# Kernel tuning notes

Hardware: AMD Instinct MI355X
Metric: run time of the kernel (lower is better)

## Reference

```python
import jax, jax.numpy as jnp
import numpy as np

P = 2; NH = 16; HS = 1024; NL = 12; NC = 1000
B, D, H, W = 32, 64, 32, 32
LFEAT = P * P * D  # 256 per-patch feature dim


def _sincos_1d(dim, pos):
    omega = np.arange(dim // 2, dtype=np.float64) / (dim / 2.0)
    omega = 1.0 / 10000 ** omega
    out = np.einsum('m,d->md', pos.reshape(-1), omega)
    return np.concatenate([np.sin(out), np.cos(out)], axis=1)


def _pos_embed(dim, grid_size):
    g = np.arange(grid_size, dtype=np.float32)
    grid = np.stack(np.meshgrid(g, g), axis=0).reshape(2, 1, grid_size, grid_size)
    emb = np.concatenate([_sincos_1d(dim // 2, grid[0]), _sincos_1d(dim // 2, grid[1])], axis=1)
    return jnp.asarray(emb, dtype=jnp.float32)


def setup_inputs() -> dict:
    key = jax.random.key(0)
    ks = iter(jax.random.split(key, 40))
    def w(shape, s=0.02):
        return jax.random.normal(next(ks), shape, jnp.float32) * s
    return {
        'x': jax.random.normal(next(ks), (B, D, H, W), jnp.float32),
        'y': jax.random.randint(next(ks), (B,), 0, NC),
        't': jax.random.randint(next(ks), (B,), 0, 1000),
        'proj_w': w((LFEAT, HS)), 'proj_b': jnp.zeros((HS,), jnp.float32),
        'pos_embed': _pos_embed(HS, H // P),
        'emb_table': w((NC + 1, HS)),
        'blk_mod_w': w((NL, HS, 6 * HS)), 'blk_mod_b': jnp.zeros((NL, 6 * HS), jnp.float32),
        'blk_wq': w((NL, HS, HS)), 'blk_bq': jnp.zeros((NL, HS), jnp.float32),
        'blk_wk': w((NL, HS, HS)), 'blk_bk': jnp.zeros((NL, HS), jnp.float32),
        'blk_wv': w((NL, HS, HS)), 'blk_bv': jnp.zeros((NL, HS), jnp.float32),
        'blk_wo': w((NL, HS, HS)), 'blk_bo': jnp.zeros((NL, HS), jnp.float32),
        'blk_fc1_w': w((NL, HS, 4 * HS)), 'blk_fc1_b': jnp.zeros((NL, 4 * HS), jnp.float32),
        'blk_fc2_w': w((NL, 4 * HS, HS)), 'blk_fc2_b': jnp.zeros((NL, HS), jnp.float32),
        'fin_mod_w': w((HS, 2 * HS)), 'fin_mod_b': jnp.zeros((2 * HS,), jnp.float32),
        'fin_out_w': w((HS, LFEAT)), 'fin_out_b': jnp.zeros((LFEAT,), jnp.float32),
    }


def _ln(z):
    mu = jnp.mean(z, -1, keepdims=True)
    var = jnp.mean((z - mu) ** 2, -1, keepdims=True)
    return (z - mu) * jax.lax.rsqrt(var + 1e-5)


def _forward(x, y, t, proj_w, proj_b, pos_embed, emb_table,
             blk_mod_w, blk_mod_b, blk_wq, blk_bq, blk_wk, blk_bk, blk_wv, blk_bv,
             blk_wo, blk_bo, blk_fc1_w, blk_fc1_b, blk_fc2_w, blk_fc2_b,
             fin_mod_w, fin_mod_b, fin_out_w, fin_out_b):
    Bc, Dc, Hc, Wc = x.shape
    Hp, Wp = Hc // P, Wc // P
    dh = HS // NH
    # patchify_flatten: (B, L, P*P*D)
    tok = x.reshape(Bc, Dc, Hp, P, Wp, P).transpose(0, 2, 4, 3, 5, 1).reshape(Bc, Hp * Wp, P * P * Dc)
    tok = tok @ proj_w + proj_b + pos_embed[None]
    # timestep_embedding: [cos, sin] order per source
    half = HS // 2
    freqs = jnp.exp(-jnp.log(jnp.float32(10000.0)) * jnp.arange(half, dtype=jnp.float32) / half)
    ang = t.astype(jnp.float32)[:, None] * freqs[None]
    c = jnp.concatenate([jnp.cos(ang), jnp.sin(ang)], axis=-1) + emb_table[y]
    c_act = jax.nn.silu(c)  # each block applies silu to c (c is not mutated across blocks)

    def block(xc, p):
        mw, mb, wq, bq, wk, bk, wv, bv, wo, bo, f1w, f1b, f2w, f2b = p
        mod = c_act @ mw + mb
        sh_a, sc_a, g_a, sh_m, sc_m, g_m = jnp.split(mod, 6, axis=1)
        hx = _ln(xc) * (1 + sc_a[:, None]) + sh_a[:, None]
        def heads(z, wz, bz):
            return (z @ wz + bz).reshape(Bc, -1, NH, dh).transpose(0, 2, 1, 3)
        q, k, v = heads(hx, wq, bq), heads(hx, wk, bk), heads(hx, wv, bv)
        logits = jnp.einsum('bhqd,bhkd->bhqk', q, k) / jnp.sqrt(jnp.float32(dh))
        # non-AR mask buffer is all zeros -> no-op
        attn = jax.nn.softmax(logits, axis=-1)
        o = jnp.einsum('bhqk,bhkd->bhqd', attn, v).transpose(0, 2, 1, 3).reshape(Bc, -1, HS)
        xc = xc + g_a[:, None] * (o @ wo + bo)
        hx = _ln(xc) * (1 + sc_m[:, None]) + sh_m[:, None]
        mlp = jax.nn.gelu(hx @ f1w + f1b, approximate=False) @ f2w + f2b
        return xc + g_m[:, None] * mlp, None

    tok, _ = jax.lax.scan(block, tok, (blk_mod_w, blk_mod_b, blk_wq, blk_bq, blk_wk, blk_bk,
                                       blk_wv, blk_bv, blk_wo, blk_bo,
                                       blk_fc1_w, blk_fc1_b, blk_fc2_w, blk_fc2_b))
    fmod = c_act @ fin_mod_w + fin_mod_b
    sh, sc = jnp.split(fmod, 2, axis=1)
    out = (_ln(tok) * (1 + sc[:, None]) + sh[:, None]) @ fin_out_w + fin_out_b
    # unpatchify -> (B, D, H, W)
    return out.reshape(Bc, Hp, Wp, P, P, Dc).transpose(0, 5, 1, 3, 2, 4).reshape(Bc, Dc, Hc, Wc)


def reference(x, y, t, proj_w, proj_b, pos_embed, emb_table,
              blk_mod_w, blk_mod_b, blk_wq, blk_bq, blk_wk, blk_bk, blk_wv, blk_bv,
              blk_wo, blk_bo, blk_fc1_w, blk_fc1_b, blk_fc2_w, blk_fc2_b,
              fin_mod_w, fin_mod_b, fin_out_w, fin_out_b):
    return _forward(x, y, t, proj_w, proj_b, pos_embed, emb_table,
                    blk_mod_w, blk_mod_b, blk_wq, blk_bq, blk_wk, blk_bk, blk_wv, blk_bv,
                    blk_wo, blk_bo, blk_fc1_w, blk_fc1_b, blk_fc2_w, blk_fc2_b,
                    fin_mod_w, fin_mod_b, fin_out_w, fin_out_b)
```

## Files before the change

kernel.cpp:

```cpp
#include <hip/hip_runtime.h>
#include <hip/hip_bf16.h>
#include <math.h>

typedef short s16x8 __attribute__((ext_vector_type(8)));
typedef float f32x4 __attribute__((ext_vector_type(4)));
typedef unsigned short u16;

#define BAR() __builtin_amdgcn_s_barrier()
#define PRIO1() __builtin_amdgcn_s_setprio(1)
#define PRIO0() __builtin_amdgcn_s_setprio(0)
#define VMCNT0() asm volatile("s_waitcnt vmcnt(0)" ::: "memory")

__device__ __forceinline__ u16 f2b(float f) {
    unsigned u = __builtin_bit_cast(unsigned, f);
    u += 0x7fffu + ((u >> 16) & 1u);
    return (u16)(u >> 16);
}
__device__ __forceinline__ f32x4 mfma16(s16x8 a, s16x8 b, f32x4 c) {
    return __builtin_amdgcn_mfma_f32_16x16x32_bf16(a, b, c, 0, 0, 0);
}
__device__ __forceinline__ void gload16(const void* g, void* l) {
    __builtin_amdgcn_global_load_lds((const __attribute__((address_space(1))) unsigned*)g,
                                     (__attribute__((address_space(3))) unsigned*)l, 16, 0, 0);
}

__global__ __launch_bounds__(256) void patchify_kernel(const float* __restrict__ x, u16* __restrict__ out) {
    int idx = blockIdx.x * 256 + threadIdx.x;
    int row = idx >> 8, col = idx & 255;
    int b = row >> 8, ll = row & 255, hp = ll >> 4, wp = ll & 15;
    int pp = col >> 6, d = col & 63;
    out[idx] = f2b(x[(size_t)((b * 64 + d) * 32 + hp * 2 + (pp >> 1)) * 32 + wp * 2 + (pp & 1)]);
}

__global__ __launch_bounds__(256) void cact_kernel(const int* __restrict__ t, const int* __restrict__ y,
                                                   const float* __restrict__ emb, float* __restrict__ cactF) {
    int b = blockIdx.x, tid = threadIdx.x;
    float tv = (float)t[b];
    int yb = y[b];
#pragma unroll
    for (int j = 0; j < 4; ++j) {
        int c = tid * 4 + j;
        int f = (c < 512) ? c : c - 512;
        float freq = __expf(-9.210340371976184f * (float)f * (1.f / 512.f));
        float ang = tv * freq;
        float v = (c < 512) ? cosf(ang) : sinf(ang);
        v += emb[(size_t)yb * 1024 + c];
        v = v / (1.f + __expf(-v));
        cactF[b * 1024 + c] = v;
    }
}

__global__ __launch_bounds__(256) void bcat_kernel(const float* __restrict__ bq, const float* __restrict__ bk,
                                                   const float* __restrict__ bv, float* __restrict__ out) {
    int lyr = blockIdx.x, j = blockIdx.y, tid = threadIdx.x;
    const float* src = (j == 0) ? bq : ((j == 1) ? bk : bv);
    float4 v = ((const float4*)(src + (size_t)lyr * 1024))[tid];
    ((float4*)(out + (size_t)lyr * 3072 + j * 1024))[tid] = v;
}

__global__ __launch_bounds__(256) void mod32_kernel(const float* __restrict__ cactF, const float* __restrict__ W,
                                                    const float* __restrict__ bias, float* __restrict__ out, int N) {
    __shared__ float cs[32 * 256];
    __shared__ float red[4 * 32 * 64];
    int tid = threadIdx.x, lane = tid & 63, kg = tid >> 6;
    int n = blockIdx.x * 64 + lane;
    float acc[32];
#pragma unroll
    for (int r = 0; r < 32; ++r) acc[r] = 0.f;
    for (int ch = 0; ch < 4; ++ch) {
        __syncthreads();
#pragma unroll
        for (int j = 0; j < 8; ++j) {
            int idx = tid * 4 + j * 1024;
            float4 v = *(const float4*)&cactF[(size_t)(idx >> 8) * 1024 + ch * 256 + (idx & 255)];
            *(float4*)&cs[idx] = v;
        }
        __syncthreads();
        const float* Wp = W + (size_t)(ch * 256 + kg * 64) * N + n;
        for (int kk = 0; kk < 64; kk += 4) {
            float w0 = Wp[(size_t)(kk + 0) * N];
            float w1 = Wp[(size_t)(kk + 1) * N];
            float w2 = Wp[(size_t)(kk + 2) * N];
            float w3 = Wp[(size_t)(kk + 3) * N];
            int kb = kg * 64 + kk;
#pragma unroll
            for (int r = 0; r < 32; ++r) {
                float4 cv = *(const float4*)&cs[r * 256 + kb];
                acc[r] += cv.x * w0 + cv.y * w1 + cv.z * w2 + cv.w * w3;
            }
        }
    }
#pragma unroll
    for (int r = 0; r < 32; ++r) red[(kg * 32 + r) * 64 + lane] = acc[r];
    __syncthreads();
    int r = tid >> 3, j0 = (tid & 7) * 8;
#pragma unroll
    for (int jj = 0; jj < 8; ++jj) {
        int nn = j0 + jj;
        float s = red[(0 * 32 + r) * 64 + nn] + red[(1 * 32 + r) * 64 + nn] +
                  red[(2 * 32 + r) * 64 + nn] + red[(3 * 32 + r) * 64 + nn];
        out[(size_t)r * N + blockIdx.x * 64 + nn] = s + bias[blockIdx.x * 64 + nn];
    }
}

__device__ __forceinline__ void tpose_body(float (*tile)[65], const float* __restrict__ in,
                                           u16* __restrict__ out, int R, int C, int r0, int c0, int tid) {
    int rr = tid >> 4, cc = (tid & 15) * 4;
#pragma unroll
    for (int j = 0; j < 4; ++j) {
        float4 v = *(const float4*)&in[(size_t)(r0 + j * 16 + rr) * C + c0 + cc];
        tile[j * 16 + rr][cc]     = v.x;
        tile[j * 16 + rr][cc + 1] = v.y;
        tile[j * 16 + rr][cc + 2] = v.z;
        tile[j * 16 + rr][cc + 3] = v.w;
    }
    __syncthreads();
    int oc = tid >> 3, r8 = (tid & 7) * 8;
#pragma unroll
    for (int j = 0; j < 2; ++j) {
        int ocl = j * 32 + oc;
        s16x8 vv;
#pragma unroll
        for (int e = 0; e < 8; ++e) vv[e] = (short)f2b(tile[r8 + e][ocl]);
        *(s16x8*)&out[(size_t)(c0 + ocl) * R + r0 + r8] = vv;
    }
}

__global__ __launch_bounds__(256) void transpose_cvt64k(const float* __restrict__ in, u16* __restrict__ out,
                                                        int R, int C) {
    __shared__ float tile[64][65];
    tpose_body(tile, in, out, R, C, blockIdx.y * 64, blockIdx.x * 64, threadIdx.x);
}

__global__ __launch_bounds__(256) void transpose_layer(
    const float* __restrict__ wq, const float* __restrict__ wk,
    const float* __restrict__ wv, const float* __restrict__ wo, const float* __restrict__ f1,
    const float* __restrict__ f2,
    u16* __restrict__ qkvT, u16* __restrict__ woT, u16* __restrict__ f1T, u16* __restrict__ f2T) {
    __shared__ float tile[64][65];
    int bid = blockIdx.x, tid = threadIdx.x;
    const float* src; u16* dst; int R, C, tloc;
    if (bid < 256)       { src = wq; dst = qkvT;               R = 1024; C = 1024; tloc = bid; }
    else if (bid < 512)  { src = wk; dst = qkvT + 1024 * 1024; R = 1024; C = 1024; tloc = bid - 256; }
    else if (bid < 768)  { src = wv; dst = qkvT + 2048 * 1024; R = 1024; C = 1024; tloc = bid - 512; }
    else if (bid < 1024) { src = wo; dst = woT;                R = 1024; C = 1024; tloc = bid - 768; }
    else if (bid < 2048) { src = f1; dst = f1T;                R = 1024; C = 4096; tloc = bid - 1024; }
    else                 { src = f2; dst = f2T;                R = 4096; C = 1024; tloc = bid - 2048; }
    int tx = C >> 6;
    int ty = tloc / tx, txi = tloc - ty * tx;
    tpose_body(tile, src, dst, R, C, ty * 64, txi * 64, tid);
}

__global__ __launch_bounds__(256) void ln_mod_kernel(const float* __restrict__ x, const float* __restrict__ modv,
                                                     int mod_ld, int sh_off, int sc_off, u16* __restrict__ out) {
    int row = blockIdx.x, tid = threadIdx.x, b = row >> 8;
    float4 xv = ((const float4*)(x + (size_t)row * 1024))[tid];
    float s = xv.x + xv.y + xv.z + xv.w;
    float s2 = xv.x * xv.x + xv.y * xv.y + xv.z * xv.z + xv.w * xv.w;
#pragma unroll
    for (int d = 1; d < 64; d <<= 1) { s += __shfl_xor(s, d); s2 += __shfl_xor(s2, d); }
    __shared__ float red[8];
    int w = tid >> 6;
    if ((tid & 63) == 0) { red[w] = s; red[4 + w] = s2; }
    __syncthreads();
    s = red[0] + red[1] + red[2] + red[3];
    s2 = red[4] + red[5] + red[6] + red[7];
    float mu = s * (1.f / 1024.f);
    float rs = rsqrtf(s2 * (1.f / 1024.f) - mu * mu + 1e-5f);
    const float* shp = modv + (size_t)b * mod_ld + sh_off;
    const float* scp = modv + (size_t)b * mod_ld + sc_off;
    float4 sh4 = ((const float4*)shp)[tid];
    float4 sc4 = ((const float4*)scp)[tid];
    u16 o0 = f2b((xv.x - mu) * rs * (1.f + sc4.x) + sh4.x);
    u16 o1 = f2b((xv.y - mu) * rs * (1.f + sc4.y) + sh4.y);
    u16 o2 = f2b((xv.z - mu) * rs * (1.f + sc4.z) + sh4.z);
    u16 o3 = f2b((xv.w - mu) * rs * (1.f + sc4.w) + sh4.w);
    unsigned long long pk = (unsigned long long)o0 | ((unsigned long long)o1 << 16) |
                            ((unsigned long long)o2 << 32) | ((unsigned long long)o3 << 48);
    *(unsigned long long*)&out[(size_t)row * 1024 + tid * 4] = pk;
}

template <int EPI>
__global__ __launch_bounds__(512, 1) void gemm8(
    const u16* __restrict__ A, int lda, const u16* __restrict__ Bt, int ldb,
    int M, int N, int K, const float* __restrict__ bias,
    float* __restrict__ outF, u16* __restrict__ outB, int ldc,
    const float* __restrict__ aux1, const float* __restrict__ aux2, int gateOff) {
    __shared__ u16 As[3][256 * 64];
    __shared__ u16 Bs[3][128 * 64];

    const int tid = threadIdx.x, w = tid >> 6, l = tid & 63;
    const int wm = w >> 1, wn = w & 1;

    const int nbn = N >> 7;
    const int orig = blockIdx.x;
    const int cpx = gridDim.x >> 3;
    const int wg = (orig & 7) * cpx + (orig >> 3);
    const int bm = wg / nbn, bn = wg - bm * nbn;
    const int row0 = bm << 8, col0 = bn << 7;

    const int NT = K >> 6;

    const int srow = tid >> 3, sslot = tid & 7;
    const int ksl = sslot ^ (srow & 7);
    const u16* gA = A + (size_t)(row0 + srow) * lda + ksl * 8;
    const u16* gB = Bt + (size_t)(col0 + srow) * ldb + ksl * 8;
    const int lOff = srow * 64 + sslot * 8;

    const int fr = l & 15, fg = l >> 4;
    const int arow = wm * 64 + fr;
    const int brow = wn * 64 + fr;

    f32x4 acc[4][4];
#pragma unroll
    for (int m = 0; m < 4; ++m)
#pragma unroll
        for (int n = 0; n < 4; ++n) acc[m][n] = (f32x4){0.f, 0.f, 0.f, 0.f};

    {
        u16* a0 = &As[0][lOff];
        u16* b0 = &Bs[0][lOff];
#pragma unroll
        for (int a = 0; a < 4; ++a) gload16(gA + (size_t)a * 64 * lda, a0 + a * 4096);
#pragma unroll
        for (int b = 0; b < 2; ++b) gload16(gB + (size_t)b * 64 * ldb, b0 + b * 4096);
        if (NT > 1) {
            u16* a1 = &As[1][lOff];
#pragma unroll
            for (int a = 0; a < 3; ++a) gload16(gA + (size_t)a * 64 * lda + 64, a1 + a * 4096);
        }
    }
    if (NT > 1) { asm volatile("s_waitcnt vmcnt(3)" ::: "memory"); }
    else        { VMCNT0(); }
    BAR();
    __builtin_amdgcn_sched_barrier(0);

    int q = 0;
    for (int t = 0; t < NT; ++t) {
        const u16* ca = As[q];
        const u16* cb = Bs[q];
        const int q1 = (q == 2) ? 0 : q + 1;
        const int q2 = (q1 == 2) ? 0 : q1 + 1;

        s16x8 af[4][2], bf[4][2];
#pragma unroll
        for (int m = 0; m < 4; ++m) {
            int r = arow + m * 16;
            af[m][0] = *(const s16x8*)(ca + r * 64 + ((fg     ^ (r & 7)) * 8));
            af[m][1] = *(const s16x8*)(ca + r * 64 + (((4 + fg) ^ (r & 7)) * 8));
        }
#pragma unroll
        for (int n = 0; n < 2; ++n) {
            int r = brow + n * 16;
            bf[n][0] = *(const s16x8*)(cb + r * 64 + ((fg     ^ (r & 7)) * 8));
            bf[n][1] = *(const s16x8*)(cb + r * 64 + (((4 + fg) ^ (r & 7)) * 8));
        }
        if (t + 1 < NT) {
            gload16(gA + (size_t)(3 * 64) * lda + (size_t)(t + 1) * 64, &As[q1][lOff] + 3 * 4096);
            gload16(gB + (size_t)(t + 1) * 64, &Bs[q1][lOff]);
            gload16(gB + (size_t)(1 * 64) * ldb + (size_t)(t + 1) * 64, &Bs[q1][lOff] + 4096);
        }
        BAR(); PRIO1();
#pragma unroll
        for (int m = 0; m < 4; ++m)
#pragma unroll
            for (int n = 0; n < 2; ++n) {
                acc[m][n] = mfma16(af[m][0], bf[n][0], acc[m][n]);
                acc[m][n] = mfma16(af[m][1], bf[n][1], acc[m][n]);
            }
        PRIO0(); BAR();
#pragma unroll
        for (int n = 0; n < 2; ++n) {
            int r = brow + (n + 2) * 16;
            bf[n + 2][0] = *(const s16x8*)(cb + r * 64 + ((fg     ^ (r & 7)) * 8));
            bf[n + 2][1] = *(const s16x8*)(cb + r * 64 + (((4 + fg) ^ (r & 7)) * 8));
        }
        if (t + 2 < NT) {
#pragma unroll
            for (int a = 0; a < 3; ++a)
                gload16(gA + (size_t)a * 64 * lda + (size_t)(t + 2) * 64, &As[q2][lOff] + a * 4096);
        }
        BAR(); PRIO1();
#pragma unroll
        for (int m = 0; m < 4; ++m)
#pragma unroll
            for (int n = 2; n < 4; ++n) {
                acc[m][n] = mfma16(af[m][0], bf[n][0], acc[m][n]);
                acc[m][n] = mfma16(af[m][1], bf[n][1], acc[m][n]);
            }
        PRIO0();
        if (t < NT - 2)       { asm volatile("s_waitcnt vmcnt(3)" ::: "memory"); }
        else if (t == NT - 2) { VMCNT0(); }
        if (t < NT - 1) {
            BAR();
            __builtin_amdgcn_sched_barrier(0);
        }
        q = q1;
    }

    const int erow = row0 + wm * 64 + fg * 4;
    const int ecol = col0 + wn * 64 + fr;
#pragma unroll
    for (int m = 0; m < 4; ++m) {
#pragma unroll
        for (int n = 0; n < 4; ++n) {
#pragma unroll
            for (int r = 0; r < 4; ++r) {
                int row = erow + m * 16 + r;
                int col = ecol + n * 16;
                float v = acc[m][n][r];
                if constexpr (EPI == 1) {
                    outB[(size_t)row * ldc + col] = f2b(v + bias[col]);
                } else if constexpr (EPI == 2) {
                    outF[(size_t)row * ldc + col] = v + bias[col] + aux1[(size_t)(row & 255) * 1024 + col];
                } else if constexpr (EPI == 3) {
                    outF[(size_t)row * ldc + col] =
                        aux1[(size_t)row * ldc + col] +
                        aux2[(size_t)(row >> 8) * 6144 + gateOff + col] * (v + bias[col]);
                } else {
                    float xg = v + bias[col];
                    outB[(size_t)row * ldc + col] = f2b(0.5f * xg * (1.f + erff(xg * 0.70710678118654752f)));
                }
            }
        }
    }
}

__global__ __launch_bounds__(256, 2) void gemm_fin(
    const u16* __restrict__ A, int lda, const u16* __restrict__ Bt, int ldb,
    int M, int N, int K, const float* __restrict__ bias, float* outF) {
    __shared__ u16 Asl[128 * 32];
    __shared__ u16 Bsl[128 * 32];
    const int tid = threadIdx.x, w = tid >> 6, l = tid & 63;
    const int row0 = blockIdx.y * 128, col0 = blockIdx.x * 128;
    const int wm = w >> 1, wn = w & 1;

    f32x4 acc[4][4];
#pragma unroll
    for (int m = 0; m < 4; ++m)
#pragma unroll
        for (int n = 0; n < 4; ++n) acc[m][n] = (f32x4){0.f, 0.f, 0.f, 0.f};

    const int rA0 = w * 16 + (l >> 2), rA1 = rA0 + 64;
    const int kc = (l & 3) * 8;
    const u16* a0 = A + (size_t)(row0 + rA0) * lda + kc;
    const u16* a1 = A + (size_t)(row0 + rA1) * lda + kc;
    const u16* b0 = Bt + (size_t)(col0 + rA0) * ldb + kc;
    const u16* b1 = Bt + (size_t)(col0 + rA1) * ldb + kc;
    u16* la0 = &Asl[rA0 * 32 + kc];
    u16* la1 = &Asl[rA1 * 32 + kc];
    u16* lb0 = &Bsl[rA0 * 32 + kc];
    u16* lb1 = &Bsl[rA1 * 32 + kc];

    for (int k0 = 0; k0 < K; k0 += 32) {
        __syncthreads();
        gload16(a0 + k0, la0);
        gload16(a1 + k0, la1);
        gload16(b0 + k0, lb0);
        gload16(b1 + k0, lb1);
        __syncthreads();
        s16x8 af[4], bfr[4];
#pragma unroll
        for (int m = 0; m < 4; ++m)
            af[m] = *(const s16x8*)&Asl[(wm * 64 + m * 16 + (l & 15)) * 32 + (l >> 4) * 8];
#pragma unroll
        for (int n = 0; n < 4; ++n)
            bfr[n] = *(const s16x8*)&Bsl[(wn * 64 + n * 16 + (l & 15)) * 32 + (l >> 4) * 8];
#pragma unroll
        for (int m = 0; m < 4; ++m)
#pragma unroll
            for (int n = 0; n < 4; ++n) acc[m][n] = mfma16(af[m], bfr[n], acc[m][n]);
    }

#pragma unroll
    for (int m = 0; m < 4; ++m) {
#pragma unroll
        for (int n = 0; n < 4; ++n) {
#pragma unroll
            for (int r = 0; r < 4; ++r) {
                int row = row0 + wm * 64 + m * 16 + (l >> 4) * 4 + r;
                int col = col0 + wn * 64 + n * 16 + (l & 15);
                float xg = acc[m][n][r] + bias[col];
                int bb = row >> 8, ll = row & 255, hp = ll >> 4, wp = ll & 15;
                int pp = col >> 6, d = col & 63;
                outF[(size_t)((bb * 64 + d) * 32 + hp * 2 + (pp >> 1)) * 32 + wp * 2 + (pp & 1)] = xg;
            }
        }
    }
}

__global__ __launch_bounds__(256, 2) void attn_kernel(const u16* __restrict__ qkv, u16* __restrict__ obuf) {
    __shared__ u16 Qs[64 * 64];
    __shared__ u16 Ks[256 * 64];
    __shared__ u16 VTs[64 * 256];
    int qt = blockIdx.x, h = blockIdx.y, b = blockIdx.z;
    int tid = threadIdx.x, w = tid >> 6, l = tid & 63;
    size_t base = (size_t)b * 256 * 3072;

    {
        int r = tid >> 2;
#pragma unroll
        for (int j = 0; j < 2; ++j) {
            int sg = (tid & 3) + j * 4;
            *(s16x8*)&Qs[r * 64 + sg * 8] =
                *(const s16x8*)&qkv[base + (size_t)(qt * 64 + r) * 3072 + h * 64 + sg * 8];
        }
    }
#pragma unroll
    for (int j = 0; j < 8; ++j) {
        int i = tid + j * 256;
        int r = i >> 3, sg = i & 7;
        *(s16x8*)&Ks[r * 64 + sg * 8] =
            *(const s16x8*)&qkv[base + (size_t)r * 3072 + 1024 + h * 64 + sg * 8];
    }
#pragma unroll
    for (int j = 0; j < 8; ++j) {
        int i = tid + j * 256;
        int r = i >> 3, sg = i & 7;
        s16x8 v = *(const s16x8*)&qkv[base + (size_t)r * 3072 + 2048 + h * 64 + sg * 8];
#pragma unroll
        for (int e = 0; e < 8; ++e) VTs[(sg * 8 + e) * 256 + r] = ((const u16*)&v)[e];
    }
    __syncthreads();

    s16x8 aq0 = *(const s16x8*)&Qs[(w * 16 + (l & 15)) * 64 + (l >> 4) * 8];
    s16x8 aq1 = *(const s16x8*)&Qs[(w * 16 + (l & 15)) * 64 + 32 + (l >> 4) * 8];
    f32x4 sf[16];
#pragma unroll
    for (int cf = 0; cf < 16; ++cf) {
        f32x4 a = (f32x4){0.f, 0.f, 0.f, 0.f};
        s16x8 bk0 = *(const s16x8*)&Ks[(cf * 16 + (l & 15)) * 64 + (l >> 4) * 8];
        s16x8 bk1 = *(const s16x8*)&Ks[(cf * 16 + (l & 15)) * 64 + 32 + (l >> 4) * 8];
        a = mfma16(aq0, bk0, a);
        a = mfma16(aq1, bk1, a);
        sf[cf] = a * 0.125f;
    }
    __syncthreads();

#pragma unroll
    for (int r = 0; r < 4; ++r) {
        float m = -1e30f;
#pragma unroll
        for (int cf = 0; cf < 16; ++cf) m = fmaxf(m, sf[cf][r]);
#pragma unroll
        for (int d = 1; d < 16; d <<= 1) m = fmaxf(m, __shfl_xor(m, d));
        float sm = 0.f;
#pragma unroll
        for (int cf = 0; cf < 16; ++cf) { float e = __expf(sf[cf][r] - m); sf[cf][r] = e; sm += e; }
#pragma unroll
        for (int d = 1; d < 16; d <<= 1) sm += __shfl_xor(sm, d);
        float inv = 1.f / sm;
        int rl = w * 16 + (l >> 4) * 4 + r;
#pragma unroll
        for (int cf = 0; cf < 16; ++cf) Ks[rl * 256 + cf * 16 + (l & 15)] = f2b(sf[cf][r] * inv);
    }
    __syncthreads();

    f32x4 oacc[4];
#pragma unroll
    for (int cf = 0; cf < 4; ++cf) oacc[cf] = (f32x4){0.f, 0.f, 0.f, 0.f};
#pragma unroll
    for (int ks = 0; ks < 8; ++ks) {
        s16x8 ap = *(const s16x8*)&Ks[(w * 16 + (l & 15)) * 256 + ks * 32 + (l >> 4) * 8];
#pragma unroll
        for (int cf = 0; cf < 4; ++cf) {
            s16x8 bv = *(const s16x8*)&VTs[(cf * 16 + (l & 15)) * 256 + ks * 32 + (l >> 4) * 8];
            oacc[cf] = mfma16(ap, bv, oacc[cf]);
        }
    }
    size_t orow0 = (size_t)(b * 256 + qt * 64 + w * 16);
#pragma unroll
    for (int cf = 0; cf < 4; ++cf)
#pragma unroll
        for (int r = 0; r < 4; ++r) {
            int rr = (l >> 4) * 4 + r;
            obuf[(orow0 + rr) * 1024 + h * 64 + cf * 16 + (l & 15)] = f2b(oacc[cf][r]);
        }
}

extern "C" void kernel_launch(void* const* d_in, const int* in_sizes, int n_in,
                              void* d_out, int out_size, void* d_ws, size_t ws_size,
                              hipStream_t stream) {
    (void)in_sizes; (void)n_in; (void)out_size; (void)ws_size;
    const float* x         = (const float*)d_in[0];
    const int*   y         = (const int*)d_in[1];
    const int*   t         = (const int*)d_in[2];
    const float* proj_w    = (const float*)d_in[3];
    const float* proj_b    = (const float*)d_in[4];
    const float* pos_embed = (const float*)d_in[5];
    const float* emb_table = (const float*)d_in[6];
    const float* blk_mod_w = (const float*)d_in[7];
    const float* blk_mod_b = (const float*)d_in[8];
    const float* blk_wq    = (const float*)d_in[9];
    const float* blk_bq    = (const float*)d_in[10];
    const float* blk_wk    = (const float*)d_in[11];
    const float* blk_bk    = (const float*)d_in[12];
    const float* blk_wv    = (const float*)d_in[13];
    const float* blk_bv    = (const float*)d_in[14];
    const float* blk_wo    = (const float*)d_in[15];
    const float* blk_bo    = (const float*)d_in[16];
    const float* blk_f1w   = (const float*)d_in[17];
    const float* blk_f1b   = (const float*)d_in[18];
    const float* blk_f2w   = (const float*)d_in[19];
    const float* blk_f2b   = (const float*)d_in[20];
    const float* fin_mod_w = (const float*)d_in[21];
    const float* fin_mod_b = (const float*)d_in[22];
    const float* fin_out_w = (const float*)d_in[23];
    const float* fin_out_b = (const float*)d_in[24];
    float* out = (float*)d_out;

    char* ws = (char*)d_ws;
    size_t off = 0;
    auto alloc = [&](size_t bytes) -> char* {
        char* p = ws + off;
        off += (bytes + 255) & ~(size_t)255;
        return p;
    };
    float* xc    = (float*)alloc(8192ull * 1024 * 4);
    u16*   hx    = (u16*)alloc(8192ull * 1024 * 2);
    u16*   qkvb  = (u16*)alloc(8192ull * 3072 * 2);
    u16*   obufp = (u16*)alloc(8192ull * 1024 * 2);
    u16*   h1    = (u16*)alloc(8192ull * 4096 * 2);
    u16*   patchA= (u16*)alloc(8192ull * 256 * 2);
    float* cactF = (float*)alloc(32ull * 1024 * 4);
    float* modb  = (float*)alloc(32ull * 6144 * 4);
    float* fmod  = (float*)alloc(32ull * 2048 * 4);
    float* bqkv  = (float*)alloc(12ull * 3072 * 4);
    u16*   projT = (u16*)alloc(1024ull * 256 * 2);
    u16*   foT   = (u16*)alloc(256ull * 1024 * 2);
    u16*   qkvT  = (u16*)alloc(3072ull * 1024 * 2);
    u16*   woT   = (u16*)alloc(1024ull * 1024 * 2);
    u16*   f1T   = (u16*)alloc(4096ull * 1024 * 2);
    u16*   f2T   = (u16*)alloc(1024ull * 4096 * 2);

    patchify_kernel<<<8192, 256, 0, stream>>>(x, patchA);
    cact_kernel<<<32, 256, 0, stream>>>(t, y, emb_table, cactF);
    bcat_kernel<<<dim3(12, 3), 256, 0, stream>>>(blk_bq, blk_bk, blk_bv, bqkv);
    transpose_cvt64k<<<dim3(16, 4), 256, 0, stream>>>(proj_w, projT, 256, 1024);
    transpose_cvt64k<<<dim3(4, 16), 256, 0, stream>>>(fin_out_w, foT, 1024, 256);
    mod32_kernel<<<32, 256, 0, stream>>>(cactF, fin_mod_w, fin_mod_b, fmod, 2048);

    gemm8<2><<<256, 512, 0, stream>>>(patchA, 256, projT, 256, 8192, 1024, 256,
                                      proj_b, xc, nullptr, 1024, pos_embed, nullptr, 0);

    for (int i = 0; i < 12; ++i) {
        transpose_layer<<<3072, 256, 0, stream>>>(
            blk_wq + (size_t)i * 1024 * 1024, blk_wk + (size_t)i * 1024 * 1024,
            blk_wv + (size_t)i * 1024 * 1024, blk_wo + (size_t)i * 1024 * 1024,
            blk_f1w + (size_t)i * 1024 * 4096, blk_f2w + (size_t)i * 4096 * 1024,
            qkvT, woT, f1T, f2T);

        mod32_kernel<<<96, 256, 0, stream>>>(cactF, blk_mod_w + (size_t)i * 1024 * 6144,
                                             blk_mod_b + (size_t)i * 6144, modb, 6144);
        ln_mod_kernel<<<8192, 256, 0, stream>>>(xc, modb, 6144, 0, 1024, hx);
        gemm8<1><<<768, 512, 0, stream>>>(hx, 1024, qkvT, 1024, 8192, 3072, 1024,
                                          bqkv + (size_t)i * 3072, nullptr, qkvb, 3072,
                                          nullptr, nullptr, 0);
        attn_kernel<<<dim3(4, 16, 32), 256, 0, stream>>>(qkvb, obufp);
        gemm8<3><<<256, 512, 0, stream>>>(obufp, 1024, woT, 1024, 8192, 1024, 1024,
                                          blk_bo + (size_t)i * 1024, xc, nullptr, 1024,
                                          xc, modb, 2048);
        ln_mod_kernel<<<8192, 256, 0, stream>>>(xc, modb, 6144, 3072, 4096, hx);
        gemm8<4><<<1024, 512, 0, stream>>>(hx, 1024, f1T, 1024, 8192, 4096, 1024,
                                           blk_f1b + (size_t)i * 4096, nullptr, h1, 4096,
                                           nullptr, nullptr, 0);
        gemm8<3><<<256, 512, 0, stream>>>(h1, 4096, f2T, 4096, 8192, 1024, 4096,
                                          blk_f2b + (size_t)i * 1024, xc, nullptr, 1024,
                                          xc, modb, 5120);
    }
    ln_mod_kernel<<<8192, 256, 0, stream>>>(xc, fmod, 2048, 0, 1024, hx);
    gemm_fin<<<dim3(2, 64), 256, 0, stream>>>(hx, 1024, foT, 1024, 8192, 256, 1024,
                                              fin_out_b, out);
}
```

Measured before the change: 5.576 ms.

## Replace 256x128 GEMM with 128x128 multi-occupancy kernel and batch weight transposes

The 512-thread 256x128x64 GEMM, with its priority-interleaved two-half schedule, is replaced by a 256-thread 128x128x32 kernel. It uses a triple-buffered global-to-LDS prefetch and launch bounds that allow 3 blocks per CU. The final-layer GEMM becomes an epilogue variant of the same kernel. All 12 layers' weight transposes now run in one upfront launch into per-layer buffers instead of one launch per layer, which removes serial per-layer transpose phases at the cost of more workspace. The smaller K-tile drops the LDS XOR swizzle, which risks bank conflicts and lower MFMA density per barrier.

```diff
diff --git a/kernel.cpp b/kernel.cpp
--- a/kernel.cpp
+++ b/kernel.cpp
@@ -7,8 +7,8 @@
 typedef unsigned short u16;
 
 #define BAR() __builtin_amdgcn_s_barrier()
-#define PRIO1() __builtin_amdgcn_s_setprio(1)
-#define PRIO0() __builtin_amdgcn_s_setprio(0)
+#define SCHEDB() __builtin_amdgcn_sched_barrier(0)
+#define VMCNT4() asm volatile("s_waitcnt vmcnt(4)" ::: "memory")
 #define VMCNT0() asm volatile("s_waitcnt vmcnt(0)" ::: "memory")
 
 __device__ __forceinline__ u16 f2b(float f) {
@@ -132,20 +132,24 @@
     tpose_body(tile, in, out, R, C, blockIdx.y * 64, blockIdx.x * 64, threadIdx.x);
 }
 
-__global__ __launch_bounds__(256) void transpose_layer(
+__global__ __launch_bounds__(256) void transpose_all(
     const float* __restrict__ wq, const float* __restrict__ wk,
-    const float* __restrict__ wv, const float* __restrict__ wo, const float* __restrict__ f1,
-    const float* __restrict__ f2,
+    const float* __restrict__ wv, const float* __restrict__ wo,
+    const float* __restrict__ f1, const float* __restrict__ f2,
     u16* __restrict__ qkvT, u16* __restrict__ woT, u16* __restrict__ f1T, u16* __restrict__ f2T) {
     __shared__ float tile[64][65];
-    int bid = blockIdx.x, tid = threadIdx.x;
+    int lyr = blockIdx.x / 3072;
+    int bid = blockIdx.x - lyr * 3072;
+    int tid = threadIdx.x;
+    const size_t sq = (size_t)lyr * 1024 * 1024;
+    const size_t sf = (size_t)lyr * 4096 * 1024;
     const float* src; u16* dst; int R, C, tloc;
-    if (bid < 256)       { src = wq; dst = qkvT;               R = 1024; C = 1024; tloc = bid; }
-    else if (bid < 512)  { src = wk; dst = qkvT + 1024 * 1024; R = 1024; C = 1024; tloc = bid - 256; }
-    else if (bid < 768)  { src = wv; dst = qkvT + 2048 * 1024; R = 1024; C = 1024; tloc = bid - 512; }
-    else if (bid < 1024) { src = wo; dst = woT;                R = 1024; C = 1024; tloc = bid - 768; }
-    else if (bid < 2048) { src = f1; dst = f1T;                R = 1024; C = 4096; tloc = bid - 1024; }
-    else                 { src = f2; dst = f2T;                R = 4096; C = 1024; tloc = bid - 2048; }
+    if (bid < 256)       { src = wq + sq; dst = qkvT + (size_t)lyr * 3072 * 1024;               R = 1024; C = 1024; tloc = bid; }
+    else if (bid < 512)  { src = wk + sq; dst = qkvT + (size_t)lyr * 3072 * 1024 + 1024 * 1024; R = 1024; C = 1024; tloc = bid - 256; }
+    else if (bid < 768)  { src = wv + sq; dst = qkvT + (size_t)lyr * 3072 * 1024 + 2048 * 1024; R = 1024; C = 1024; tloc = bid - 512; }
+    else if (bid < 1024) { src = wo + sq; dst = woT + sq;                                       R = 1024; C = 1024; tloc = bid - 768; }
+    else if (bid < 2048) { src = f1 + sf; dst = f1T + sf;                                       R = 1024; C = 4096; tloc = bid - 1024; }
+    else                 { src = f2 + sf; dst = f2T + sf;                                       R = 4096; C = 1024; tloc = bid - 2048; }
     int tx = C >> 6;
     int ty = tloc / tx, txi = tloc - ty * tx;
     tpose_body(tile, src, dst, R, C, ty * 64, txi * 64, tid);
@@ -181,35 +185,31 @@
 }
 
 template <int EPI>
-__global__ __launch_bounds__(512, 1) void gemm8(
+__global__ __launch_bounds__(256, 3) void gemm128p(
     const u16* __restrict__ A, int lda, const u16* __restrict__ Bt, int ldb,
     int M, int N, int K, const float* __restrict__ bias,
     float* __restrict__ outF, u16* __restrict__ outB, int ldc,
     const float* __restrict__ aux1, const float* __restrict__ aux2, int gateOff) {
-    __shared__ u16 As[3][256 * 64];
-    __shared__ u16 Bs[3][128 * 64];
+    __shared__ u16 As[3][128 * 32];
+    __shared__ u16 Bs[3][128 * 32];
 
     const int tid = threadIdx.x, w = tid >> 6, l = tid & 63;
     const int wm = w >> 1, wn = w & 1;
 
     const int nbn = N >> 7;
-    const int orig = blockIdx.x;
     const int cpx = gridDim.x >> 3;
-    const int wg = (orig & 7) * cpx + (orig >> 3);
+    const int wg = (blockIdx.x & 7) * cpx + (blockIdx.x >> 3);
     const int bm = wg / nbn, bn = wg - bm * nbn;
-    const int row0 = bm << 8, col0 = bn << 7;
-
-    const int NT = K >> 6;
-
-    const int srow = tid >> 3, sslot = tid & 7;
-    const int ksl = sslot ^ (srow & 7);
-    const u16* gA = A + (size_t)(row0 + srow) * lda + ksl * 8;
-    const u16* gB = Bt + (size_t)(col0 + srow) * ldb + ksl * 8;
-    const int lOff = srow * 64 + sslot * 8;
-
-    const int fr = l & 15, fg = l >> 4;
-    const int arow = wm * 64 + fr;
-    const int brow = wn * 64 + fr;
+    const int row0 = bm << 7, col0 = bn << 7;
+    const int NT = K >> 5;
+
+    const int rA0 = w * 16 + (l >> 2), rA1 = rA0 + 64;
+    const int kc = (l & 3) * 8;
+    const u16* a0 = A + (size_t)(row0 + rA0) * lda + kc;
+    const u16* a1 = A + (size_t)(row0 + rA1) * lda + kc;
+    const u16* b0 = Bt + (size_t)(col0 + rA0) * ldb + kc;
+    const u16* b1 = Bt + (size_t)(col0 + rA1) * ldb + kc;
+    const int lo0 = rA0 * 32 + kc, lo1 = rA1 * 32 + kc;
 
     f32x4 acc[4][4];
 #pragma unroll
@@ -217,97 +217,50 @@
 #pragma unroll
         for (int n = 0; n < 4; ++n) acc[m][n] = (f32x4){0.f, 0.f, 0.f, 0.f};
 
-    {
-        u16* a0 = &As[0][lOff];
-        u16* b0 = &Bs[0][lOff];
-#pragma unroll
-        for (int a = 0; a < 4; ++a) gload16(gA + (size_t)a * 64 * lda, a0 + a * 4096);
-#pragma unroll
-        for (int b = 0; b < 2; ++b) gload16(gB + (size_t)b * 64 * ldb, b0 + b * 4096);
-        if (NT > 1) {
-            u16* a1 = &As[1][lOff];
-#pragma unroll
-            for (int a = 0; a < 3; ++a) gload16(gA + (size_t)a * 64 * lda + 64, a1 + a * 4096);
-        }
-    }
-    if (NT > 1) { asm volatile("s_waitcnt vmcnt(3)" ::: "memory"); }
-    else        { VMCNT0(); }
-    BAR();
-    __builtin_amdgcn_sched_barrier(0);
+    gload16(a0, &As[0][lo0]); gload16(a1, &As[0][lo1]);
+    gload16(b0, &Bs[0][lo0]); gload16(b1, &Bs[0][lo1]);
+    if (NT > 1) {
+        gload16(a0 + 32, &As[1][lo0]); gload16(a1 + 32, &As[1][lo1]);
+        gload16(b0 + 32, &Bs[1][lo0]); gload16(b1 + 32, &Bs[1][lo1]);
+        VMCNT4();
+    } else {
+        VMCNT0();
+    }
+    BAR(); SCHEDB();
 
     int q = 0;
     for (int t = 0; t < NT; ++t) {
-        const u16* ca = As[q];
-        const u16* cb = Bs[q];
-        const int q1 = (q == 2) ? 0 : q + 1;
-        const int q2 = (q1 == 2) ? 0 : q1 + 1;
-
-        s16x8 af[4][2], bf[4][2];
-#pragma unroll
-        for (int m = 0; m < 4; ++m) {
-            int r = arow + m * 16;
-            af[m][0] = *(const s16x8*)(ca + r * 64 + ((fg     ^ (r & 7)) * 8));
-            af[m][1] = *(const s16x8*)(ca + r * 64 + (((4 + fg) ^ (r & 7)) * 8));
-        }
-#pragma unroll
-        for (int n = 0; n < 2; ++n) {
-            int r = brow + n * 16;
-            bf[n][0] = *(const s16x8*)(cb + r * 64 + ((fg     ^ (r & 7)) * 8));
-            bf[n][1] = *(const s16x8*)(cb + r * 64 + (((4 + fg) ^ (r & 7)) * 8));
-        }
-        if (t + 1 < NT) {
-            gload16(gA + (size_t)(3 * 64) * lda + (size_t)(t + 1) * 64, &As[q1][lOff] + 3 * 4096);
-            gload16(gB + (size_t)(t + 1) * 64, &Bs[q1][lOff]);
-            gload16(gB + (size_t)(1 * 64) * ldb + (size_t)(t + 1) * 64, &Bs[q1][lOff] + 4096);
-        }
-        BAR(); PRIO1();
+        int q2 = q + 2; if (q2 >= 3) q2 -= 3;
+        if (t + 2 < NT) {
+            int k2 = (t + 2) * 32;
+            gload16(a0 + k2, &As[q2][lo0]); gload16(a1 + k2, &As[q2][lo1]);
+            gload16(b0 + k2, &Bs[q2][lo0]); gload16(b1 + k2, &Bs[q2][lo1]);
+        }
+        s16x8 af[4], bfr[4];
 #pragma unroll
         for (int m = 0; m < 4; ++m)
-#pragma unroll
-            for (int n = 0; n < 2; ++n) {
-                acc[m][n] = mfma16(af[m][0], bf[n][0], acc[m][n]);
-                acc[m][n] = mfma16(af[m][1], bf[n][1], acc[m][n]);
-            }
-        PRIO0(); BAR();
-#pragma unroll
-        for (int n = 0; n < 2; ++n) {
-            int r = brow + (n + 2) * 16;
-            bf[n + 2][0] = *(const s16x8*)(cb + r * 64 + ((fg     ^ (r & 7)) * 8));
-            bf[n + 2][1] = *(const s16x8*)(cb + r * 64 + (((4 + fg) ^ (r & 7)) * 8));
-        }
-        if (t + 2 < NT) {
-#pragma unroll
-            for (int a = 0; a < 3; ++a)
-                gload16(gA + (size_t)a * 64 * lda + (size_t)(t + 2) * 64, &As[q2][lOff] + a * 4096);
-        }
-        BAR(); PRIO1();
+            af[m] = *(const s16x8*)&As[q][(wm * 64 + m * 16 + (l & 15)) * 32 + (l >> 4) * 8];
+#pragma unroll
+        for (int n = 0; n < 4; ++n)
+            bfr[n] = *(const s16x8*)&Bs[q][(wn * 64 + n * 16 + (l & 15)) * 32 + (l >> 4) * 8];
 #pragma unroll
         for (int m = 0; m < 4; ++m)
 #pragma unroll
-            for (int n = 2; n < 4; ++n) {
-                acc[m][n] = mfma16(af[m][0], bf[n][0], acc[m][n]);
-                acc[m][n] = mfma16(af[m][1], bf[n][1], acc[m][n]);
-            }
-        PRIO0();
-        if (t < NT - 2)       { asm volatile("s_waitcnt vmcnt(3)" ::: "memory"); }
-        else if (t == NT - 2) { VMCNT0(); }
-        if (t < NT - 1) {
-            BAR();
-            __builtin_amdgcn_sched_barrier(0);
-        }
-        q = q1;
-    }
-
-    const int erow = row0 + wm * 64 + fg * 4;
-    const int ecol = col0 + wn * 64 + fr;
+            for (int n = 0; n < 4; ++n) acc[m][n] = mfma16(af[m], bfr[n], acc[m][n]);
+        if (t + 2 < NT)      { VMCNT4(); }
+        else if (t + 1 < NT) { VMCNT0(); }
+        if (t + 1 < NT) { BAR(); SCHEDB(); }
+        q = q + 1; if (q >= 3) q -= 3;
+    }
+
 #pragma unroll
     for (int m = 0; m < 4; ++m) {
 #pragma unroll
         for (int n = 0; n < 4; ++n) {
 #pragma unroll
             for (int r = 0; r < 4; ++r) {
-                int row = erow + m * 16 + r;
-                int col = ecol + n * 16;
+                int row = row0 + wm * 64 + m * 16 + (l >> 4) * 4 + r;
+                int col = col0 + wn * 64 + n * 16 + (l & 15);
                 float v = acc[m][n][r];
                 if constexpr (EPI == 1) {
                     outB[(size_t)row * ldc + col] = f2b(v + bias[col]);
@@ -317,73 +270,15 @@
                     outF[(size_t)row * ldc + col] =
                         aux1[(size_t)row * ldc + col] +
                         aux2[(size_t)(row >> 8) * 6144 + gateOff + col] * (v + bias[col]);
+                } else if constexpr (EPI == 4) {
+                    float xg = v + bias[col];
+                    outB[(size_t)row * ldc + col] = f2b(0.5f * xg * (1.f + erff(xg * 0.70710678118654752f)));
                 } else {
                     float xg = v + bias[col];
-                    outB[(size_t)row * ldc + col] = f2b(0.5f * xg * (1.f + erff(xg * 0.70710678118654752f)));
+                    int bb = row >> 8, ll = row & 255, hp = ll >> 4, wp = ll & 15;
+                    int pp = col >> 6, d = col & 63;
+                    outF[(size_t)((bb * 64 + d) * 32 + hp * 2 + (pp >> 1)) * 32 + wp * 2 + (pp & 1)] = xg;
                 }
-            }
-        }
-    }
-}
-
-__global__ __launch_bounds__(256, 2) void gemm_fin(
-    const u16* __restrict__ A, int lda, const u16* __restrict__ Bt, int ldb,
-    int M, int N, int K, const float* __restrict__ bias, float* outF) {
-    __shared__ u16 Asl[128 * 32];
-    __shared__ u16 Bsl[128 * 32];
-    const int tid = threadIdx.x, w = tid >> 6, l = tid & 63;
-    const int row0 = blockIdx.y * 128, col0 = blockIdx.x * 128;
-    const int wm = w >> 1, wn = w & 1;
-
-    f32x4 acc[4][4];
-#pragma unroll
-    for (int m = 0; m < 4; ++m)
-#pragma unroll
-        for (int n = 0; n < 4; ++n) acc[m][n] = (f32x4){0.f, 0.f, 0.f, 0.f};
-
-    const int rA0 = w * 16 + (l >> 2), rA1 = rA0 + 64;
-    const int kc = (l & 3) * 8;
-    const u16* a0 = A + (size_t)(row0 + rA0) * lda + kc;
-    const u16* a1 = A + (size_t)(row0 + rA1) * lda + kc;
-    const u16* b0 = Bt + (size_t)(col0 + rA0) * ldb + kc;
-    const u16* b1 = Bt + (size_t)(col0 + rA1) * ldb + kc;
-    u16* la0 = &Asl[rA0 * 32 + kc];
-    u16* la1 = &Asl[rA1 * 32 + kc];
-    u16* lb0 = &Bsl[rA0 * 32 + kc];
-    u16* lb1 = &Bsl[rA1 * 32 + kc];
-
-    for (int k0 = 0; k0 < K; k0 += 32) {
-        __syncthreads();
-        gload16(a0 + k0, la0);
-        gload16(a1 + k0, la1);
-        gload16(b0 + k0, lb0);
-        gload16(b1 + k0, lb1);
-        __syncthreads();
-        s16x8 af[4], bfr[4];
-#pragma unroll
-        for (int m = 0; m < 4; ++m)
-            af[m] = *(const s16x8*)&Asl[(wm * 64 + m * 16 + (l & 15)) * 32 + (l >> 4) * 8];
-#pragma unroll
-        for (int n = 0; n < 4; ++n)
-            bfr[n] = *(const s16x8*)&Bsl[(wn * 64 + n * 16 + (l & 15)) * 32 + (l >> 4) * 8];
-#pragma unroll
-        for (int m = 0; m < 4; ++m)
-#pragma unroll
-            for (int n = 0; n < 4; ++n) acc[m][n] = mfma16(af[m], bfr[n], acc[m][n]);
-    }
-
-#pragma unroll
-    for (int m = 0; m < 4; ++m) {
-#pragma unroll
-        for (int n = 0; n < 4; ++n) {
-#pragma unroll
-            for (int r = 0; r < 4; ++r) {
-                int row = row0 + wm * 64 + m * 16 + (l >> 4) * 4 + r;
-                int col = col0 + wn * 64 + n * 16 + (l & 15);
-                float xg = acc[m][n][r] + bias[col];
-                int bb = row >> 8, ll = row & 255, hp = ll >> 4, wp = ll & 15;
-                int pp = col >> 6, d = col & 63;
-                outF[(size_t)((bb * 64 + d) * 32 + hp * 2 + (pp >> 1)) * 32 + wp * 2 + (pp & 1)] = xg;
             }
         }
     }
@@ -528,10 +423,10 @@
     float* bqkv  = (float*)alloc(12ull * 3072 * 4);
     u16*   projT = (u16*)alloc(1024ull * 256 * 2);
     u16*   foT   = (u16*)alloc(256ull * 1024 * 2);
-    u16*   qkvT  = (u16*)alloc(3072ull * 1024 * 2);
-    u16*   woT   = (u16*)alloc(1024ull * 1024 * 2);
-    u16*   f1T   = (u16*)alloc(4096ull * 1024 * 2);
-    u16*   f2T   = (u16*)alloc(1024ull * 4096 * 2);
+    u16*   qkvTa = (u16*)alloc(12ull * 3072 * 1024 * 2);
+    u16*   woTa  = (u16*)alloc(12ull * 1024 * 1024 * 2);
+    u16*   f1Ta  = (u16*)alloc(12ull * 4096 * 1024 * 2);
+    u16*   f2Ta  = (u16*)alloc(12ull * 1024 * 4096 * 2);
 
     patchify_kernel<<<8192, 256, 0, stream>>>(x, patchA);
     cact_kernel<<<32, 256, 0, stream>>>(t, y, emb_table, cactF);
@@ -539,36 +434,37 @@
     transpose_cvt64k<<<dim3(16, 4), 256, 0, stream>>>(proj_w, projT, 256, 1024);
     transpose_cvt64k<<<dim3(4, 16), 256, 0, stream>>>(fin_out_w, foT, 1024, 256);
     mod32_kernel<<<32, 256, 0, stream>>>(cactF, fin_mod_w, fin_mod_b, fmod, 2048);
-
-    gemm8<2><<<256, 512, 0, stream>>>(patchA, 256, projT, 256, 8192, 1024, 256,
-                                      proj_b, xc, nullptr, 1024, pos_embed, nullptr, 0);
+    transpose_all<<<12 * 3072, 256, 0, stream>>>(blk_wq, blk_wk, blk_wv, blk_wo,
+                                                 blk_f1w, blk_f2w, qkvTa, woTa, f1Ta, f2Ta);
+
+    gemm128p<2><<<512, 256, 0, stream>>>(patchA, 256, projT, 256, 8192, 1024, 256,
+                                         proj_b, xc, nullptr, 1024, pos_embed, nullptr, 0);
 
     for (int i = 0; i < 12; ++i) {
-        transpose_layer<<<3072, 256, 0, stream>>>(
-            blk_wq + (size_t)i * 1024 * 1024, blk_wk + (size_t)i * 1024 * 1024,
-            blk_wv + (size_t)i * 1024 * 1024, blk_wo + (size_t)i * 1024 * 1024,
-            blk_f1w + (size_t)i * 1024 * 4096, blk_f2w + (size_t)i * 4096 * 1024,
-            qkvT, woT, f1T, f2T);
+        const u16* qkvT = qkvTa + (size_t)i * 3072 * 1024;
+        const u16* woT  = woTa + (size_t)i * 1024 * 1024;
+        const u16* f1T  = f1Ta + (size_t)i * 4096 * 1024;
+        const u16* f2T  = f2Ta + (size_t)i * 4096 * 1024;
 
         mod32_kernel<<<96, 256, 0, stream>>>(cactF, blk_mod_w + (size_t)i * 1024 * 6144,
                                              blk_mod_b + (size_t)i * 6144, modb, 6144);
         ln_mod_kernel<<<8192, 256, 0, stream>>>(xc, modb, 6144, 0, 1024, hx);
-        gemm8<1><<<768, 512, 0, stream>>>(hx, 1024, qkvT, 1024, 8192, 3072, 1024,
-                                          bqkv + (size_t)i * 3072, nullptr, qkvb, 3072,
-                                          nullptr, nullptr, 0);
+        gemm128p<1><<<1536, 256, 0, stream>>>(hx, 1024, qkvT, 1024, 8192, 3072, 1024,
+                                              bqkv + (size_t)i * 3072, nullptr, qkvb, 3072,
+                                              nullptr, nullptr, 0);
         attn_kernel<<<dim3(4, 16, 32), 256, 0, stream>>>(qkvb, obufp);
-        gemm8<3><<<256, 512, 0, stream>>>(obufp, 1024, woT, 1024, 8192, 1024, 1024,
-                                          blk_bo + (size_t)i * 1024, xc, nullptr, 1024,
-                                          xc, modb, 2048);
+        gemm128p<3><<<512, 256, 0, stream>>>(obufp, 1024, woT, 1024, 8192, 1024, 1024,
+                                             blk_bo + (size_t)i * 1024, xc, nullptr, 1024,
+                                             xc, modb, 2048);
         ln_mod_kernel<<<8192, 256, 0, stream>>>(xc, modb, 6144, 3072, 4096, hx);
-        gemm8<4><<<1024, 512, 0, stream>>>(hx, 1024, f1T, 1024, 8192, 4096, 1024,
-                                           blk_f1b + (size_t)i * 4096, nullptr, h1, 4096,
-                                           nullptr, nullptr, 0);
-        gemm8<3><<<256, 512, 0, stream>>>(h1, 4096, f2T, 4096, 8192, 1024, 4096,
-                                          blk_f2b + (size_t)i * 1024, xc, nullptr, 1024,
-                                          xc, modb, 5120);
+        gemm128p<4><<<2048, 256, 0, stream>>>(hx, 1024, f1T, 1024, 8192, 4096, 1024,
+                                              blk_f1b + (size_t)i * 4096, nullptr, h1, 4096,
+                                              nullptr, nullptr, 0);
+        gemm128p<3><<<512, 256, 0, stream>>>(h1, 4096, f2T, 4096, 8192, 1024, 4096,
+                                             blk_f2b + (size_t)i * 1024, xc, nullptr, 1024,
+                                             xc, modb, 5120);
     }
     ln_mod_kernel<<<8192, 256, 0, stream>>>(xc, fmod, 2048, 0, 1024, hx);
-    gemm_fin<<<dim3(2, 64), 256, 0, stream>>>(hx, 1024, foT, 1024, 8192, 256, 1024,
-                                              fin_out_b, out);
-}
+    gemm128p<5><<<128, 256, 0, stream>>>(hx, 1024, foT, 1024, 8192, 256, 1024,
+                                         fin_out_b, out, nullptr, 256, nullptr, nullptr, 0);
+}
```

Measured after the change: 6.149 ms. 1.1x slower.
